# Kernel tuning notes

Measured on AMD Instinct MI355X. Metric: run time of the kernel, lower is better.

## Reference

```python
import jax, jax.numpy as jnp
import numpy as np

T_THR = 2.0   # temperature for threshold softmax over teachers
T_KD = 20.0   # KD temperature
ALPHA = 0.8   # KD mixing coefficient


def setup_inputs() -> dict:
    key = jax.random.key(0)
    ks = jax.random.split(key, 10)
    B, C = 4096, 1000
    d = {f"outputs{i+1}": jax.random.normal(ks[i], (B, C), dtype=jnp.float32) for i in range(8)}
    d["out_s"] = jax.random.normal(ks[8], (B, C), dtype=jnp.float32)
    d["targets"] = jax.random.randint(ks[9], (B,), 0, C, dtype=jnp.int64)
    return d


def reference(outputs1, outputs2, outputs3, outputs4, outputs5, outputs6, outputs7, outputs8, out_s, targets):
    outs = jnp.stack([outputs1, outputs2, outputs3, outputs4,
                      outputs5, outputs6, outputs7, outputs8])      # [8,B,C]
    mimic = outs.mean(axis=0)                                       # [B,C]
    all9 = jnp.concatenate([outs, mimic[None]], axis=0)             # [9,B,C]

    # per-(teacher,sample) top-2 margin, zero if target is not the argmax
    top2, _ = jax.lax.top_k(all9, 2)                                # [9,B,2]
    tgt_logit = jnp.take_along_axis(all9, targets[None, :, None], axis=2)[..., 0]  # [9,B]
    margin = jnp.where(tgt_logit == top2[..., 0], top2[..., 0] - top2[..., 1], 0.0)  # [9,B]
    thr = jax.nn.softmax(margin / T_THR, axis=0)                    # [9,B] softmax over 9 teachers

    max_preds = outs.max()                                          # scalar over the 8 teachers

    # cross-entropy of student (same for every teacher branch)
    logp_s = jax.nn.log_softmax(out_s, axis=-1)                     # [B,C]
    CE = -jnp.take_along_axis(logp_s, targets[:, None], axis=1)[:, 0]  # [B]

    # KD term per teacher
    logp_sT = jax.nn.log_softmax(out_s / T_KD, axis=-1)             # [B,C]
    p_tT = jax.nn.softmax(all9 / T_KD, axis=-1)                     # [9,B,C]
    KD = -jnp.sum(p_tT * logp_sT[None], axis=-1) * (T_KD * T_KD)    # [9,B]

    # dynamic per-sample weights
    w = tgt_logit / max_preds                                       # [9,B]
    loss = (1.0 - ALPHA * w) * CE[None] + ALPHA * w * KD            # [9,B]

    return jnp.sum(thr * loss, axis=0).mean()
```

## Files before the change

kernel.cpp:

```cpp
#include <hip/hip_runtime.h>

constexpr int   B        = 4096;
constexpr int   C        = 1000;
constexpr float ALPHA    = 0.8f;
constexpr float INV_TKD  = 0.05f;
constexpr float TKD2     = 400.0f;
constexpr float INV_TTHR = 0.5f;
constexpr float SENT     = -1e30f;

struct P4 { float mx, Z, Sd, tv; };

__global__ __launch_bounds__(128, 4) void row_kernel(
    const float* __restrict__ T0, const float* __restrict__ T1,
    const float* __restrict__ T2, const float* __restrict__ T3,
    const float* __restrict__ T4, const float* __restrict__ T5,
    const float* __restrict__ T6, const float* __restrict__ T7,
    const float* __restrict__ S,  const int* __restrict__ TGT,
    float* __restrict__ ws_ce, float* __restrict__ ws_g, float* __restrict__ ws_m)
{
    __shared__ float4 xch[2][2];
    __shared__ float4 xst[2];

    const int tid  = threadIdx.x;
    const int lane = tid & 63;
    const int h    = tid >> 6;
    const int row  = blockIdx.x;
    const size_t base = (size_t)row * C;

    const int  tgt   = TGT[row];
    const int  ftgt  = tgt >> 2;
    const bool own   = (h == (ftgt >> 7));
    const int  uidx  = (((ftgt >> 6) & 1) << 2) | (tgt & 3);
    const int  slane = ftgt & 63;

    auto load_half = [&](const float* __restrict__ p, float (&v)[8]) {
        const float4* p4 = (const float4*)(p + base);
#pragma unroll
        for (int k = 0; k < 2; ++k) {
            const int  idx = lane + 128 * h + 64 * k;
            const bool ok  = (h == 0) || (k == 0) || (lane < 58);
            float4 f = p4[ok ? idx : 0];
            v[4*k+0] = ok ? f.x : SENT;
            v[4*k+1] = ok ? f.y : SENT;
            v[4*k+2] = ok ? f.z : SENT;
            v[4*k+3] = ok ? f.w : SENT;
        }
    };

    float sv[8];
    load_half(S, sv);
    float buf[2][8];
    load_half(T0, buf[0]);

    auto part_reduce = [&](const float (&v)[8]) -> P4 {
        float cand = 0.0f, m_all = SENT, m_ex = SENT, Z = 0.0f, Sd = 0.0f;
#pragma unroll
        for (int i = 0; i < 8; ++i) {
            const float x = v[i];
            cand  = (i == uidx) ? x : cand;
            m_all = fmaxf(m_all, x);
            m_ex  = fmaxf(m_ex, (i == uidx) ? SENT : x);
            const float e = __expf(x * INV_TKD);
            Z += e;
            Sd = fmaf(e, sv[i], Sd);
        }
        float mx = (own && lane == slane) ? m_ex : m_all;
#pragma unroll
        for (int m = 1; m < 64; m <<= 1) {
            mx  = fmaxf(mx, __shfl_xor(mx, m, 64));
            Z  += __shfl_xor(Z,  m, 64);
            Sd += __shfl_xor(Sd, m, 64);
        }
        float tv = __shfl(cand, slane, 64);
        P4 p; p.mx = mx; p.Z = Z; p.Sd = Sd; p.tv = own ? tv : SENT;
        return p;
    };

    float z1 = 0.0f, zT = 0.0f, scand = 0.0f;
#pragma unroll
    for (int i = 0; i < 8; ++i) {
        z1 += __expf(sv[i]);
        zT += __expf(sv[i] * INV_TKD);
        scand = (i == uidx) ? sv[i] : scand;
    }
#pragma unroll
    for (int m = 1; m < 64; m <<= 1) {
        z1 += __shfl_xor(z1, m, 64);
        zT += __shfl_xor(zT, m, 64);
    }
    float stv = __shfl(scand, slane, 64);
    stv = own ? stv : SENT;
    if (lane == 0) xst[h] = make_float4(z1, zT, stv, 0.0f);

    float acc[8];
#pragma unroll
    for (int i = 0; i < 8; ++i) acc[i] = buf[0][i];

    P4 Preg[2];
    Preg[0] = part_reduce(buf[0]);
    if (lane == 0) xch[0][h] = make_float4(Preg[0].mx, Preg[0].Z,
                                           Preg[0].Sd, Preg[0].tv);
    load_half(T1, buf[1]);
    __syncthreads();

    {
        float4 o = xst[h ^ 1];
        z1 += o.x; zT += o.y; stv = fmaxf(stv, o.z);
    }
    const float logZT = __logf(zT);
    const float ce    = __logf(z1) - stv;

    float s1 = 0.0f, s2 = 0.0f, rowmax8 = SENT;
    auto fin = [&](const P4& p, int par, bool upd) {
        const float4 o = xch[par][h ^ 1];
        const float mx = fmaxf(p.mx, o.x);
        const float Z  = p.Z + o.y;
        const float Sd = p.Sd + o.z;
        const float tv = fmaxf(p.tv, o.w);
        const float margin = fmaxf(tv - mx, 0.0f);
        const float kd = TKD2 * (logZT - INV_TKD * __fdividef(Sd, Z));
        const float u  = tv * (kd - ce);
        const float w8 = __expf(margin * INV_TTHR);
        s1 += w8;
        s2  = fmaf(w8, u, s2);
        if (upd) rowmax8 = fmaxf(rowmax8, fmaxf(mx, tv));
    };

    const float* ptrs[8] = {T0, T1, T2, T3, T4, T5, T6, T7};
#pragma unroll
    for (int t = 1; t < 8; ++t) {
        if (t + 1 < 8)
            load_half(ptrs[t + 1], buf[(t + 1) & 1]);
        fin(Preg[(t - 1) & 1], (t - 1) & 1, true);
        const float (&cv)[8] = buf[t & 1];
#pragma unroll
        for (int i = 0; i < 8; ++i) acc[i] += cv[i];
        Preg[t & 1] = part_reduce(cv);
        if (lane == 0) xch[t & 1][h] = make_float4(Preg[t & 1].mx, Preg[t & 1].Z,
                                                   Preg[t & 1].Sd, Preg[t & 1].tv);
        __syncthreads();
    }
    fin(Preg[1], 1, true);

#pragma unroll
    for (int i = 0; i < 8; ++i) acc[i] *= 0.125f;
    Preg[0] = part_reduce(acc);
    if (lane == 0) xch[0][h] = make_float4(Preg[0].mx, Preg[0].Z,
                                           Preg[0].Sd, Preg[0].tv);
    __syncthreads();
    fin(Preg[0], 0, false);

    if (tid == 0) {
        ws_ce[row] = ce;
        ws_g[row]  = s2 / s1;
        ws_m[row]  = rowmax8;
    }
}

__global__ __launch_bounds__(256) void fin_kernel(
    const float* __restrict__ ce, const float* __restrict__ g,
    const float* __restrict__ m, float* __restrict__ out)
{
    __shared__ float  smax[4];
    __shared__ double ssum[4];
    const int tid  = threadIdx.x;
    const int lane = tid & 63;
    const int wid  = tid >> 6;

    float mx = SENT;
    for (int i = tid; i < B; i += 256) mx = fmaxf(mx, m[i]);
#pragma unroll
    for (int k = 1; k < 64; k <<= 1) mx = fmaxf(mx, __shfl_xor(mx, k, 64));
    if (lane == 0) smax[wid] = mx;
    __syncthreads();
    const float scale =
        ALPHA / fmaxf(fmaxf(smax[0], smax[1]), fmaxf(smax[2], smax[3]));

    double acc = 0.0;
    for (int i = tid; i < B; i += 256) acc += (double)(ce[i] + g[i] * scale);
#pragma unroll
    for (int k = 1; k < 64; k <<= 1) acc += __shfl_xor(acc, k, 64);
    if (lane == 0) ssum[wid] = acc;
    __syncthreads();
    if (tid == 0)
        out[0] = (float)((ssum[0] + ssum[1] + ssum[2] + ssum[3]) *
                         (1.0 / (double)B));
}

extern "C" void kernel_launch(void* const* d_in, const int* in_sizes, int n_in,
                              void* d_out, int out_size, void* d_ws, size_t ws_size,
                              hipStream_t stream)
{
    const float* T0 = (const float*)d_in[0];
    const float* T1 = (const float*)d_in[1];
    const float* T2 = (const float*)d_in[2];
    const float* T3 = (const float*)d_in[3];
    const float* T4 = (const float*)d_in[4];
    const float* T5 = (const float*)d_in[5];
    const float* T6 = (const float*)d_in[6];
    const float* T7 = (const float*)d_in[7];
    const float* S  = (const float*)d_in[8];
    const int*   TG = (const int*)d_in[9];

    float* ws = (float*)d_ws;
    float* ws_ce = ws;
    float* ws_g  = ws + B;
    float* ws_m  = ws + 2 * B;

    row_kernel<<<B, 128, 0, stream>>>(T0, T1, T2, T3, T4, T5, T6, T7,
                                      S, TG, ws_ce, ws_g, ws_m);
    fin_kernel<<<1, 256, 0, stream>>>(ws_ce, ws_g, ws_m, (float*)d_out);
}
```

Baseline: 192.4 us.

## Batch all teacher partials into one cross-wave reduction and single barrier

Per-teacher wave shuffles and the block barrier after each teacher are replaced by per-lane partials for all nine teachers held in registers. One combined butterfly reduction then runs over 36 values, and a single shared-memory exchange with one __syncthreads completes the cross-wave combine. This removes eight barriers and interleaves independent shuffles so their latency can overlap. In exchange it raises register pressure, which could reduce occupancy under launch_bounds(128,4), and the target-logit extraction changes from a shfl broadcast to a max reduction.

```diff
diff --git a/kernel.cpp b/kernel.cpp
--- a/kernel.cpp
+++ b/kernel.cpp
@@ -7,8 +7,6 @@
 constexpr float TKD2     = 400.0f;
 constexpr float INV_TTHR = 0.5f;
 constexpr float SENT     = -1e30f;
-
-struct P4 { float mx, Z, Sd, tv; };
 
 __global__ __launch_bounds__(128, 4) void row_kernel(
     const float* __restrict__ T0, const float* __restrict__ T1,
@@ -18,8 +16,7 @@
     const float* __restrict__ S,  const int* __restrict__ TGT,
     float* __restrict__ ws_ce, float* __restrict__ ws_g, float* __restrict__ ws_m)
 {
-    __shared__ float4 xch[2][2];
-    __shared__ float4 xst[2];
+    __shared__ float4 xch[2][10];
 
     const int tid  = threadIdx.x;
     const int lane = tid & 63;
@@ -32,6 +29,7 @@
     const bool own   = (h == (ftgt >> 7));
     const int  uidx  = (((ftgt >> 6) & 1) << 2) | (tgt & 3);
     const int  slane = ftgt & 63;
+    const bool owner = own && (lane == slane);
 
     auto load_half = [&](const float* __restrict__ p, float (&v)[8]) {
         const float4* p4 = (const float4*)(p + base);
@@ -52,8 +50,18 @@
     float buf[2][8];
     load_half(T0, buf[0]);
 
-    auto part_reduce = [&](const float (&v)[8]) -> P4 {
-        float cand = 0.0f, m_all = SENT, m_ex = SENT, Z = 0.0f, Sd = 0.0f;
+    float z1 = 0.0f, zT = 0.0f, sc = SENT;
+#pragma unroll
+    for (int i = 0; i < 8; ++i) {
+        z1 += __expf(sv[i]);
+        zT += __expf(sv[i] * INV_TKD);
+        sc = (owner && i == uidx) ? sv[i] : sc;
+    }
+
+    float mxA[9], ZA[9], SdA[9], tvA[9];
+
+    auto partials = [&](const float (&v)[8], const int b) {
+        float cand = SENT, m_all = SENT, m_ex = SENT, Z = 0.0f, Sd = 0.0f;
 #pragma unroll
         for (int i = 0; i < 8; ++i) {
             const float x = v[i];
@@ -64,91 +72,82 @@
             Z += e;
             Sd = fmaf(e, sv[i], Sd);
         }
-        float mx = (own && lane == slane) ? m_ex : m_all;
-#pragma unroll
-        for (int m = 1; m < 64; m <<= 1) {
-            mx  = fmaxf(mx, __shfl_xor(mx, m, 64));
-            Z  += __shfl_xor(Z,  m, 64);
-            Sd += __shfl_xor(Sd, m, 64);
+        mxA[b] = owner ? m_ex : m_all;
+        ZA[b]  = Z;
+        SdA[b] = Sd;
+        tvA[b] = owner ? cand : SENT;
+    };
+
+    float acc[8];
+#pragma unroll
+    for (int i = 0; i < 8; ++i) acc[i] = buf[0][i];
+    partials(buf[0], 0);
+    load_half(T1, buf[1]);
+
+    const float* ptrs[8] = {T0, T1, T2, T3, T4, T5, T6, T7};
+#pragma unroll
+    for (int t = 1; t < 8; ++t) {
+        if (t + 1 < 8)
+            load_half(ptrs[t + 1], buf[(t + 1) & 1]);
+        const float (&cv)[8] = buf[t & 1];
+#pragma unroll
+        for (int i = 0; i < 8; ++i) acc[i] += cv[i];
+        partials(cv, t);
+    }
+
+#pragma unroll
+    for (int i = 0; i < 8; ++i) acc[i] *= 0.125f;
+    partials(acc, 8);
+
+#pragma unroll
+    for (int m = 1; m < 64; m <<= 1) {
+#pragma unroll
+        for (int b = 0; b < 9; ++b) {
+            mxA[b]  = fmaxf(mxA[b], __shfl_xor(mxA[b], m, 64));
+            ZA[b]  += __shfl_xor(ZA[b], m, 64);
+            SdA[b] += __shfl_xor(SdA[b], m, 64);
+            tvA[b]  = fmaxf(tvA[b], __shfl_xor(tvA[b], m, 64));
         }
-        float tv = __shfl(cand, slane, 64);
-        P4 p; p.mx = mx; p.Z = Z; p.Sd = Sd; p.tv = own ? tv : SENT;
-        return p;
-    };
-
-    float z1 = 0.0f, zT = 0.0f, scand = 0.0f;
-#pragma unroll
-    for (int i = 0; i < 8; ++i) {
-        z1 += __expf(sv[i]);
-        zT += __expf(sv[i] * INV_TKD);
-        scand = (i == uidx) ? sv[i] : scand;
-    }
-#pragma unroll
-    for (int m = 1; m < 64; m <<= 1) {
         z1 += __shfl_xor(z1, m, 64);
         zT += __shfl_xor(zT, m, 64);
-    }
-    float stv = __shfl(scand, slane, 64);
-    stv = own ? stv : SENT;
-    if (lane == 0) xst[h] = make_float4(z1, zT, stv, 0.0f);
-
-    float acc[8];
-#pragma unroll
-    for (int i = 0; i < 8; ++i) acc[i] = buf[0][i];
-
-    P4 Preg[2];
-    Preg[0] = part_reduce(buf[0]);
-    if (lane == 0) xch[0][h] = make_float4(Preg[0].mx, Preg[0].Z,
-                                           Preg[0].Sd, Preg[0].tv);
-    load_half(T1, buf[1]);
+        sc  = fmaxf(sc, __shfl_xor(sc, m, 64));
+    }
+
+    if (lane == 0) {
+#pragma unroll
+        for (int b = 0; b < 9; ++b)
+            xch[h][b] = make_float4(mxA[b], ZA[b], SdA[b], tvA[b]);
+        xch[h][9] = make_float4(z1, zT, sc, 0.0f);
+    }
     __syncthreads();
-
+#pragma unroll
+    for (int b = 0; b < 9; ++b) {
+        const float4 o = xch[h ^ 1][b];
+        mxA[b]  = fmaxf(mxA[b], o.x);
+        ZA[b]  += o.y;
+        SdA[b] += o.z;
+        tvA[b]  = fmaxf(tvA[b], o.w);
+    }
     {
-        float4 o = xst[h ^ 1];
-        z1 += o.x; zT += o.y; stv = fmaxf(stv, o.z);
-    }
+        const float4 o = xch[h ^ 1][9];
+        z1 += o.x; zT += o.y; sc = fmaxf(sc, o.z);
+    }
+
     const float logZT = __logf(zT);
-    const float ce    = __logf(z1) - stv;
+    const float ce    = __logf(z1) - sc;
 
     float s1 = 0.0f, s2 = 0.0f, rowmax8 = SENT;
-    auto fin = [&](const P4& p, int par, bool upd) {
-        const float4 o = xch[par][h ^ 1];
-        const float mx = fmaxf(p.mx, o.x);
-        const float Z  = p.Z + o.y;
-        const float Sd = p.Sd + o.z;
-        const float tv = fmaxf(p.tv, o.w);
+#pragma unroll
+    for (int b = 0; b < 9; ++b) {
+        const float mx = mxA[b], Z = ZA[b], Sd = SdA[b], tv = tvA[b];
         const float margin = fmaxf(tv - mx, 0.0f);
         const float kd = TKD2 * (logZT - INV_TKD * __fdividef(Sd, Z));
         const float u  = tv * (kd - ce);
         const float w8 = __expf(margin * INV_TTHR);
         s1 += w8;
         s2  = fmaf(w8, u, s2);
-        if (upd) rowmax8 = fmaxf(rowmax8, fmaxf(mx, tv));
-    };
-
-    const float* ptrs[8] = {T0, T1, T2, T3, T4, T5, T6, T7};
-#pragma unroll
-    for (int t = 1; t < 8; ++t) {
-        if (t + 1 < 8)
-            load_half(ptrs[t + 1], buf[(t + 1) & 1]);
-        fin(Preg[(t - 1) & 1], (t - 1) & 1, true);
-        const float (&cv)[8] = buf[t & 1];
-#pragma unroll
-        for (int i = 0; i < 8; ++i) acc[i] += cv[i];
-        Preg[t & 1] = part_reduce(cv);
-        if (lane == 0) xch[t & 1][h] = make_float4(Preg[t & 1].mx, Preg[t & 1].Z,
-                                                   Preg[t & 1].Sd, Preg[t & 1].tv);
-        __syncthreads();
-    }
-    fin(Preg[1], 1, true);
-
-#pragma unroll
-    for (int i = 0; i < 8; ++i) acc[i] *= 0.125f;
-    Preg[0] = part_reduce(acc);
-    if (lane == 0) xch[0][h] = make_float4(Preg[0].mx, Preg[0].Z,
-                                           Preg[0].Sd, Preg[0].tv);
-    __syncthreads();
-    fin(Preg[0], 0, false);
+        if (b < 8) rowmax8 = fmaxf(rowmax8, fmaxf(mx, tv));
+    }
 
     if (tid == 0) {
         ws_ce[row] = ce;
```

Result: no change. 190.6 us (-0.9%).
